# Kernel tuning notes

Measured on AMD Instinct MI355X. Metric: run time of the kernel, lower is better.

The kernel has to match this reference:

```python
import jax, jax.numpy as jnp
import numpy as np

N_NODES = 50000
N_EDGES = 250000
NODE_DIM = 32
EDGE_DIM = 16
HIDDEN = 32


def setup_inputs() -> dict:
    key = jax.random.key(0)
    ks = jax.random.split(key, 12)
    s = lambda *d: 1.0 / np.sqrt(d[0])
    return {
        "x": jax.random.normal(ks[0], (N_NODES, NODE_DIM), jnp.float32),
        "edge_index": jax.random.randint(ks[1], (2, N_EDGES), 0, N_NODES, jnp.int64),
        "edge_attr": jax.random.normal(ks[2], (N_EDGES, EDGE_DIM), jnp.float32),
        # edge_network: Linear(edge_dim, hidden) -> ReLU -> Linear(hidden, node_dim*hidden)
        "w1": jax.random.normal(ks[3], (EDGE_DIM, HIDDEN), jnp.float32) * s(EDGE_DIM),
        "b1": jnp.zeros((HIDDEN,), jnp.float32),
        "w2": jax.random.normal(ks[4], (HIDDEN, NODE_DIM * HIDDEN), jnp.float32) * s(HIDDEN),
        "b2": jnp.zeros((NODE_DIM * HIDDEN,), jnp.float32),
        # NNConv root weight + bias (root_weight=True, bias=True defaults)
        "root": jax.random.normal(ks[5], (NODE_DIM, HIDDEN), jnp.float32) * s(NODE_DIM),
        "bias_conv": jnp.zeros((HIDDEN,), jnp.float32),
        # node_network: Linear(node_dim + hidden, hidden) -> ReLU (dropout=0)
        "w3": jax.random.normal(ks[6], (NODE_DIM + HIDDEN, HIDDEN), jnp.float32) * s(NODE_DIM + HIDDEN),
        "b3": jnp.zeros((HIDDEN,), jnp.float32),
    }


def reference(x, edge_index, edge_attr, w1, b1, w2, b2, root, bias_conv, w3, b3):
    src, dst = edge_index[0], edge_index[1]  # j -> i (source_to_target)
    # per-edge dynamic weight matrices [E, node_dim, hidden]
    h = jax.nn.relu(edge_attr @ w1 + b1)
    W = (h @ w2 + b2).reshape(-1, NODE_DIM, HIDDEN)
    msg = jnp.einsum("ed,edh->eh", x[src], W)
    # mean aggregation by target node
    agg = jax.ops.segment_sum(msg, dst, num_segments=N_NODES)
    cnt = jax.ops.segment_sum(jnp.ones((msg.shape[0],), msg.dtype), dst, num_segments=N_NODES)
    agg = agg / jnp.maximum(cnt, 1.0)[:, None]
    messages = agg + x @ root + bias_conv
    combined = jnp.concatenate([x, messages], axis=-1)
    return jax.nn.relu(combined @ w3 + b3)
```

## Files before the change

kernel.cpp:

```cpp
#include <hip/hip_runtime.h>

#define NN 50000
#define NE 250000
#define NT 7813

typedef __attribute__((ext_vector_type(8)))  short    s16x8;
typedef __attribute__((ext_vector_type(16))) float    f32x16;
typedef __attribute__((ext_vector_type(4)))  unsigned u32x4;

__device__ __forceinline__ unsigned bf16r(float f) {
    unsigned u = __float_as_uint(f);
    return (u + 0x7fffu + ((u >> 16) & 1u)) >> 16;
}
__device__ __forceinline__ short bfs(float f) {
    __bf16 b = (__bf16)f;
    return __builtin_bit_cast(short, b);
}

__global__ void pack_w2(const float* __restrict__ w2, const float* __restrict__ b2,
                        unsigned* __restrict__ w2pk) {
    int i = blockIdx.x * 256 + threadIdx.x;
    if (i >= 66 * 256) return;
    int s = i >> 8, l = (i >> 2) & 63, q = i & 3;
    int col = l & 31;
    int kk = s * 16 + (l >> 5) * 8 + 2 * q;
    float f0 = (kk < 1024) ? w2[(kk >> 5) * 1024 + (kk & 31) * 32 + col]
                           : b2[(kk - 1024) * 32 + col];
    int kk1 = kk + 1;
    float f1 = (kk1 < 1024) ? w2[(kk1 >> 5) * 1024 + (kk1 & 31) * 32 + col]
                            : b2[(kk1 - 1024) * 32 + col];
    w2pk[i] = (bf16r(f1) << 16) | bf16r(f0);
}

__global__ __launch_bounds__(1024, 4) void edge_kernel(
    const float* __restrict__ x, const int* __restrict__ ei,
    const float* __restrict__ ea, const float* __restrict__ w1,
    const float* __restrict__ b1, const unsigned* __restrict__ w2pk,
    float* __restrict__ agg, float* __restrict__ cnt)
{
    extern __shared__ char smem[];
    unsigned* sw2 = (unsigned*)smem;
    {
        u32x4* dstp = (u32x4*)sw2;
        const u32x4* srcp = (const u32x4*)w2pk;
        for (int c = threadIdx.x; c < 66 * 64; c += 1024) dstp[c] = srcp[c];
    }
    __syncthreads();

    const int lane = threadIdx.x & 63;
    const int wave = threadIdx.x >> 6;
    const int er0  = lane & 31;
    const int half = lane >> 5;
    float* hl = (float*)(smem + 66 * 1024) + wave * (32 * 33);

    s16x8 w1f;
    #pragma unroll
    for (int j = 0; j < 8; j++) w1f[j] = bfs(w1[(half * 8 + j) * 32 + er0]);
    const float b1v = b1[er0];

    for (int tile = blockIdx.x * 16 + wave; tile < NT; tile += gridDim.x * 16) {
        const int B0  = tile * 32;
        const int eg  = B0 + er0;
        const int egc = eg < NE ? eg : NE - 1;
        const int src = ei[egc];

        const float* xp = x + src * 32 + half * 8;
        float4 xa = *(const float4*)xp;
        float4 xb = *(const float4*)(xp + 4);
        float4 xc = *(const float4*)(xp + 16);
        float4 xd = *(const float4*)(xp + 20);
        float xlo[8] = {xa.x, xa.y, xa.z, xa.w, xb.x, xb.y, xb.z, xb.w};
        float xhi[8] = {xc.x, xc.y, xc.z, xc.w, xd.x, xd.y, xd.z, xd.w};

        const float* epp = ea + (size_t)egc * 16 + half * 8;
        float4 e0 = *(const float4*)epp;
        float4 e1 = *(const float4*)(epp + 4);
        s16x8 eaf;
        eaf[0]=bfs(e0.x); eaf[1]=bfs(e0.y); eaf[2]=bfs(e0.z); eaf[3]=bfs(e0.w);
        eaf[4]=bfs(e1.x); eaf[5]=bfs(e1.y); eaf[6]=bfs(e1.z); eaf[7]=bfs(e1.w);

        f32x16 hc = {};
        hc = __builtin_amdgcn_mfma_f32_32x32x16_bf16(eaf, w1f, hc, 0, 0, 0);
        #pragma unroll
        for (int r = 0; r < 16; r++) {
            int e = (r & 3) + 8 * (r >> 2) + 4 * half;
            hl[e * 33 + er0] = fmaxf(hc[r] + b1v, 0.f);
        }

        f32x16 acc = {};
        const float* hrow = hl + er0 * 33;
        #pragma unroll
        for (int s2 = 0; s2 < 32; s2++) {
            float hk = hrow[s2];
            s16x8 alo, ahi;
            #pragma unroll
            for (int j = 0; j < 8; j++) alo[j] = bfs(hk * xlo[j]);
            #pragma unroll
            for (int j = 0; j < 8; j++) ahi[j] = bfs(hk * xhi[j]);
            s16x8 blo = *(const s16x8*)(sw2 + (2 * s2)     * 256 + lane * 4);
            s16x8 bhi = *(const s16x8*)(sw2 + (2 * s2 + 1) * 256 + lane * 4);
            acc = __builtin_amdgcn_mfma_f32_32x32x16_bf16(alo, blo, acc, 0, 0, 0);
            acc = __builtin_amdgcn_mfma_f32_32x32x16_bf16(ahi, bhi, acc, 0, 0, 0);
        }
        {
            s16x8 alo, ahi;
            #pragma unroll
            for (int j = 0; j < 8; j++) alo[j] = bfs(xlo[j]);
            #pragma unroll
            for (int j = 0; j < 8; j++) ahi[j] = bfs(xhi[j]);
            s16x8 b64 = *(const s16x8*)(sw2 + 64 * 256 + lane * 4);
            s16x8 b65 = *(const s16x8*)(sw2 + 65 * 256 + lane * 4);
            acc = __builtin_amdgcn_mfma_f32_32x32x16_bf16(alo, b64, acc, 0, 0, 0);
            acc = __builtin_amdgcn_mfma_f32_32x32x16_bf16(ahi, b65, acc, 0, 0, 0);
        }

        #pragma unroll
        for (int r = 0; r < 16; r++) {
            int e  = (r & 3) + 8 * (r >> 2) + 4 * half;
            int ge = B0 + e;
            if (ge < NE) {
                int d = ei[NE + ge];
                atomicAdd(&agg[d * 32 + er0], acc[r]);
            }
        }
        if (lane < 32 && eg < NE) atomicAdd(&cnt[ei[NE + eg]], 1.0f);
    }
}

__global__ __launch_bounds__(256) void node_kernel(
    const float* __restrict__ x, const float* __restrict__ root,
    const float* __restrict__ bias_conv, const float* __restrict__ w3,
    const float* __restrict__ b3, const float* __restrict__ cnt,
    float* __restrict__ out)
{
    __shared__ float xs[8][32];
    __shared__ float ms[8][32];
    const int li = threadIdx.x >> 5, hid = threadIdx.x & 31;
    const int n = blockIdx.x * 8 + li;

    xs[li][hid] = x[n * 32 + hid];
    __syncthreads();

    float xr = 0.f;
    #pragma unroll
    for (int t = 0; t < 32; t++) xr += xs[li][t] * root[t * 32 + hid];

    float c = cnt[n];
    float ic = 1.0f / fmaxf(c, 1.0f);
    float m = out[n * 32 + hid] * ic + xr + bias_conv[hid];
    ms[li][hid] = m;
    __syncthreads();

    float o = b3[hid];
    #pragma unroll
    for (int t = 0; t < 32; t++) {
        o += xs[li][t] * w3[t * 32 + hid];
        o += ms[li][t] * w3[(32 + t) * 32 + hid];
    }
    out[n * 32 + hid] = fmaxf(o, 0.f);
}

extern "C" void kernel_launch(void* const* d_in, const int* in_sizes, int n_in,
                              void* d_out, int out_size, void* d_ws, size_t ws_size,
                              hipStream_t stream) {
    const float* x    = (const float*)d_in[0];
    const int*   ei   = (const int*)  d_in[1];
    const float* ea   = (const float*)d_in[2];
    const float* w1   = (const float*)d_in[3];
    const float* b1   = (const float*)d_in[4];
    const float* w2   = (const float*)d_in[5];
    const float* b2   = (const float*)d_in[6];
    const float* root = (const float*)d_in[7];
    const float* bc   = (const float*)d_in[8];
    const float* w3   = (const float*)d_in[9];
    const float* b3   = (const float*)d_in[10];

    float*    out  = (float*)d_out;
    float*    cnt  = (float*)d_ws;
    unsigned* w2pk = (unsigned*)((char*)d_ws + NN * sizeof(float));

    hipMemsetAsync(d_out, 0, (size_t)NN * 32 * sizeof(float), stream);
    hipMemsetAsync(cnt,   0, (size_t)NN * sizeof(float), stream);

    pack_w2<<<66, 256, 0, stream>>>(w2, b2, w2pk);

    const int lds_bytes = 66 * 1024 + 16 * 32 * 33 * 4;
    hipFuncSetAttribute((const void*)edge_kernel,
                        hipFuncAttributeMaxDynamicSharedMemorySize, lds_bytes);
    edge_kernel<<<256, 1024, lds_bytes, stream>>>(x, ei, ea, w1, b1, w2pk, out, cnt);

    node_kernel<<<NN / 8, 256, 0, stream>>>(x, root, bc, w3, b3, cnt, out);
}
```

Baseline: 86.10 us.

## Split edge-network hidden dim across block pairs and fuse zeroing into prep kernel

Each edge tile is now handled by two blocks, each covering half of the 32 hidden units. Each block keeps only half of the packed w2 in static LDS, and the hidden activations move between lane halves with shuffles instead of going through an LDS scratch buffer. The two memsets and the w2 packing are merged into one prep kernel, and blocks shrink to 512 threads with higher occupancy. The cost is that x gathers, edge_attr loads and the first-layer MFMA are done twice, and every message still issues the full set of float atomics, so atomic traffic to agg doubles.

After: 246.2 us. +186.0%, slower.

```diff
diff --git a/kernel.cpp b/kernel.cpp
--- a/kernel.cpp
+++ b/kernel.cpp
@@ -3,6 +3,7 @@
 #define NN 50000
 #define NE 250000
 #define NT 7813
+#define NBH 768
 
 typedef __attribute__((ext_vector_type(8)))  short    s16x8;
 typedef __attribute__((ext_vector_type(16))) float    f32x16;
@@ -17,33 +18,44 @@
     return __builtin_bit_cast(short, b);
 }
 
-__global__ void pack_w2(const float* __restrict__ w2, const float* __restrict__ b2,
-                        unsigned* __restrict__ w2pk) {
-    int i = blockIdx.x * 256 + threadIdx.x;
-    if (i >= 66 * 256) return;
-    int s = i >> 8, l = (i >> 2) & 63, q = i & 3;
-    int col = l & 31;
-    int kk = s * 16 + (l >> 5) * 8 + 2 * q;
-    float f0 = (kk < 1024) ? w2[(kk >> 5) * 1024 + (kk & 31) * 32 + col]
-                           : b2[(kk - 1024) * 32 + col];
-    int kk1 = kk + 1;
-    float f1 = (kk1 < 1024) ? w2[(kk1 >> 5) * 1024 + (kk1 & 31) * 32 + col]
-                            : b2[(kk1 - 1024) * 32 + col];
-    w2pk[i] = (bf16r(f1) << 16) | bf16r(f0);
-}
-
-__global__ __launch_bounds__(1024, 4) void edge_kernel(
+__global__ __launch_bounds__(256) void prep_kernel(
+    const float* __restrict__ w2, const float* __restrict__ b2,
+    unsigned* __restrict__ w2pk, float* __restrict__ agg,
+    float* __restrict__ cnt)
+{
+    int g = blockIdx.x * 256 + threadIdx.x;
+    if (g < 16896) {
+        int kh = g / 8448, rem = g % 8448;
+        int s = rem >> 8, l = (rem >> 2) & 63, q = rem & 3;
+        int S = (s < 32) ? 32 * kh + s : 64 + kh;
+        int col = l & 31;
+        int kk = S * 16 + (l >> 5) * 8 + 2 * q;
+        float f0 = (kk < 1024) ? w2[(kk >> 5) * 1024 + (kk & 31) * 32 + col]
+                               : b2[(kk - 1024) * 32 + col];
+        int k1 = kk + 1;
+        float f1 = (k1 < 1024) ? w2[(k1 >> 5) * 1024 + (k1 & 31) * 32 + col]
+                               : b2[(k1 - 1024) * 32 + col];
+        w2pk[g] = (bf16r(f1) << 16) | bf16r(f0);
+    } else {
+        int c = g - 16896;
+        if (c < 400000)      ((float4*)agg)[c]          = float4{0.f,0.f,0.f,0.f};
+        else if (c < 412500) ((float4*)cnt)[c - 400000] = float4{0.f,0.f,0.f,0.f};
+    }
+}
+
+__global__ __launch_bounds__(512, 6) void edge_kernel(
     const float* __restrict__ x, const int* __restrict__ ei,
     const float* __restrict__ ea, const float* __restrict__ w1,
     const float* __restrict__ b1, const unsigned* __restrict__ w2pk,
     float* __restrict__ agg, float* __restrict__ cnt)
 {
-    extern __shared__ char smem[];
-    unsigned* sw2 = (unsigned*)smem;
+    __shared__ unsigned sw2[33 * 256];
+    const int kh    = blockIdx.x & 1;
+    const int bslot = blockIdx.x >> 1;
     {
+        const u32x4* srcp = (const u32x4*)(w2pk + kh * 8448);
         u32x4* dstp = (u32x4*)sw2;
-        const u32x4* srcp = (const u32x4*)w2pk;
-        for (int c = threadIdx.x; c < 66 * 64; c += 1024) dstp[c] = srcp[c];
+        for (int c = threadIdx.x; c < 2112; c += 512) dstp[c] = srcp[c];
     }
     __syncthreads();
 
@@ -51,14 +63,18 @@
     const int wave = threadIdx.x >> 6;
     const int er0  = lane & 31;
     const int half = lane >> 5;
-    float* hl = (float*)(smem + 66 * 1024) + wave * (32 * 33);
 
     s16x8 w1f;
     #pragma unroll
     for (int j = 0; j < 8; j++) w1f[j] = bfs(w1[(half * 8 + j) * 32 + er0]);
-    const float b1v = b1[er0];
-
-    for (int tile = blockIdx.x * 16 + wave; tile < NT; tile += gridDim.x * 16) {
+    float b1r[8];
+    #pragma unroll
+    for (int i = 0; i < 8; i++)
+        b1r[i] = b1[16 * kh + (i & 3) + 8 * (i >> 2) + 4 * half];
+
+    const int ws0 = ((bslot * 8 + wave) + kh * (NBH * 4)) % (NBH * 8);
+
+    for (int tile = ws0; tile < NT; tile += NBH * 8) {
         const int B0  = tile * 32;
         const int eg  = B0 + er0;
         const int egc = eg < NE ? eg : NE - 1;
@@ -80,38 +96,59 @@
         eaf[4]=bfs(e1.x); eaf[5]=bfs(e1.y); eaf[6]=bfs(e1.z); eaf[7]=bfs(e1.w);
 
         f32x16 hc = {};
-        hc = __builtin_amdgcn_mfma_f32_32x32x16_bf16(eaf, w1f, hc, 0, 0, 0);
+        hc = __builtin_amdgcn_mfma_f32_32x32x16_bf16(w1f, eaf, hc, 0, 0, 0);
+
+        float X8[8];
+        if (kh == 0) {
+            #pragma unroll
+            for (int i = 0; i < 8; i++) X8[i] = fmaxf(hc[i]     + b1r[i], 0.f);
+        } else {
+            #pragma unroll
+            for (int i = 0; i < 8; i++) X8[i] = fmaxf(hc[8 + i] + b1r[i], 0.f);
+        }
+
+        f32x16 acc = {};
         #pragma unroll
-        for (int r = 0; r < 16; r++) {
-            int e = (r & 3) + 8 * (r >> 2) + 4 * half;
-            hl[e * 33 + er0] = fmaxf(hc[r] + b1v, 0.f);
-        }
-
-        f32x16 acc = {};
-        const float* hrow = hl + er0 * 33;
-        #pragma unroll
-        for (int s2 = 0; s2 < 32; s2++) {
-            float hk = hrow[s2];
-            s16x8 alo, ahi;
-            #pragma unroll
-            for (int j = 0; j < 8; j++) alo[j] = bfs(hk * xlo[j]);
-            #pragma unroll
-            for (int j = 0; j < 8; j++) ahi[j] = bfs(hk * xhi[j]);
-            s16x8 blo = *(const s16x8*)(sw2 + (2 * s2)     * 256 + lane * 4);
-            s16x8 bhi = *(const s16x8*)(sw2 + (2 * s2 + 1) * 256 + lane * 4);
-            acc = __builtin_amdgcn_mfma_f32_32x32x16_bf16(alo, blo, acc, 0, 0, 0);
-            acc = __builtin_amdgcn_mfma_f32_32x32x16_bf16(ahi, bhi, acc, 0, 0, 0);
+        for (int i = 0; i < 8; i++) {
+            const float other = __shfl_xor(X8[i], 32);
+            const float hA = half ? other : X8[i];
+            const float hB = half ? X8[i] : other;
+            const int kA = (i & 3) + 8 * (i >> 2);
+            {
+                s16x8 alo, ahi;
+                #pragma unroll
+                for (int j = 0; j < 8; j++) alo[j] = bfs(hA * xlo[j]);
+                #pragma unroll
+                for (int j = 0; j < 8; j++) ahi[j] = bfs(hA * xhi[j]);
+                s16x8 blo = *(const s16x8*)(sw2 + (2 * kA)     * 256 + lane * 4);
+                s16x8 bhi = *(const s16x8*)(sw2 + (2 * kA + 1) * 256 + lane * 4);
+                acc = __builtin_amdgcn_mfma_f32_32x32x16_bf16(alo, blo, acc, 0, 0, 0);
+                acc = __builtin_amdgcn_mfma_f32_32x32x16_bf16(ahi, bhi, acc, 0, 0, 0);
+            }
+            {
+                const int kB = kA + 4;
+                s16x8 alo, ahi;
+                #pragma unroll
+                for (int j = 0; j < 8; j++) alo[j] = bfs(hB * xlo[j]);
+                #pragma unroll
+                for (int j = 0; j < 8; j++) ahi[j] = bfs(hB * xhi[j]);
+                s16x8 blo = *(const s16x8*)(sw2 + (2 * kB)     * 256 + lane * 4);
+                s16x8 bhi = *(const s16x8*)(sw2 + (2 * kB + 1) * 256 + lane * 4);
+                acc = __builtin_amdgcn_mfma_f32_32x32x16_bf16(alo, blo, acc, 0, 0, 0);
+                acc = __builtin_amdgcn_mfma_f32_32x32x16_bf16(ahi, bhi, acc, 0, 0, 0);
+            }
         }
         {
-            s16x8 alo, ahi;
-            #pragma unroll
-            for (int j = 0; j < 8; j++) alo[j] = bfs(xlo[j]);
-            #pragma unroll
-            for (int j = 0; j < 8; j++) ahi[j] = bfs(xhi[j]);
-            s16x8 b64 = *(const s16x8*)(sw2 + 64 * 256 + lane * 4);
-            s16x8 b65 = *(const s16x8*)(sw2 + 65 * 256 + lane * 4);
-            acc = __builtin_amdgcn_mfma_f32_32x32x16_bf16(alo, b64, acc, 0, 0, 0);
-            acc = __builtin_amdgcn_mfma_f32_32x32x16_bf16(ahi, b65, acc, 0, 0, 0);
+            s16x8 ab;
+            if (kh == 0) {
+                #pragma unroll
+                for (int j = 0; j < 8; j++) ab[j] = bfs(xlo[j]);
+            } else {
+                #pragma unroll
+                for (int j = 0; j < 8; j++) ab[j] = bfs(xhi[j]);
+            }
+            s16x8 bb = *(const s16x8*)(sw2 + 32 * 256 + lane * 4);
+            acc = __builtin_amdgcn_mfma_f32_32x32x16_bf16(ab, bb, acc, 0, 0, 0);
         }
 
         #pragma unroll
@@ -123,7 +160,8 @@
                 atomicAdd(&agg[d * 32 + er0], acc[r]);
             }
         }
-        if (lane < 32 && eg < NE) atomicAdd(&cnt[ei[NE + eg]], 1.0f);
+        if (kh == 0 && lane < 32 && eg < NE)
+            atomicAdd(&cnt[ei[NE + eg]], 1.0f);
     }
 }
 
@@ -179,15 +217,9 @@
     float*    cnt  = (float*)d_ws;
     unsigned* w2pk = (unsigned*)((char*)d_ws + NN * sizeof(float));
 
-    hipMemsetAsync(d_out, 0, (size_t)NN * 32 * sizeof(float), stream);
-    hipMemsetAsync(cnt,   0, (size_t)NN * sizeof(float), stream);
-
-    pack_w2<<<66, 256, 0, stream>>>(w2, b2, w2pk);
-
-    const int lds_bytes = 66 * 1024 + 16 * 32 * 33 * 4;
-    hipFuncSetAttribute((const void*)edge_kernel,
-                        hipFuncAttributeMaxDynamicSharedMemorySize, lds_bytes);
-    edge_kernel<<<256, 1024, lds_bytes, stream>>>(x, ei, ea, w1, b1, w2pk, out, cnt);
+    prep_kernel<<<1678, 256, 0, stream>>>(w2, b2, w2pk, out, cnt);
+
+    edge_kernel<<<2 * NBH, 512, 0, stream>>>(x, ei, ea, w1, b1, w2pk, out, cnt);
 
     node_kernel<<<NN / 8, 256, 0, stream>>>(x, root, bc, w3, b3, cnt, out);
 }
```
